# Performance work log

Hardware: AMD Instinct MI355X
Metric: run time of the kernel (lower is better)

## Reference

```python
import jax, jax.numpy as jnp
import numpy as np

EPS = 1e-5

def _bn(x, g, b):
    # training-mode BatchNorm3d over (N, T, H, W) per channel (axis=1), biased variance
    red = (0, 2, 3, 4)
    m = x.mean(red, keepdims=True)
    v = x.var(red, keepdims=True)
    s = (1, -1, 1, 1, 1)
    return (x - m) / jnp.sqrt(v + EPS) * g.reshape(s) + b.reshape(s)

def _conv3d(x, w, b):
    # Conv3d kernel (1,3,3), padding (0,1,1)
    y = jax.lax.conv_general_dilated(x, w, (1, 1, 1), ((0, 0), (1, 1), (1, 1)),
                                     dimension_numbers=('NCDHW', 'OIDHW', 'NCDHW'))
    return y + b[None, :, None, None, None]

def _forward(x1, x2, attn_weight, W_up, b_up, W_mlp, b_mlp, g_mlp, be_mlp,
             W_c1, b_c1, g_c1, be_c1, W_c2, b_c2, g_c2, be_c2):
    w2 = W_up[:, :, 0]  # [Cin, Cout, 2, 2]
    y = jnp.einsum('bcthw,cokl->bothkwl', x1, w2)
    b_, o, t, h, k, w_, l = y.shape
    x1u = y.reshape(b_, o, t, h * k, w_ * l) + b_up[None, :, None, None, None]

    bs, d_in, T, H, W = x2.shape
    nH = attn_weight.shape[0]
    hh, ww = attn_weight.shape[2], attn_weight.shape[3]
    # [nH, bs, h, w, T, T] -> [nH*bs, T*T, h, w], bilinear upsample to (H, W)
    A = attn_weight.transpose(0, 1, 4, 5, 2, 3).reshape(nH * bs, T * T, hh, ww)
    A = jax.image.resize(A, (nH * bs, T * T, H, W), method='linear')
    A = A.reshape(nH, bs, T, T, H, W)
    # per-(head,b,H,W) temporal attention matmul: avoids materializing x2.repeat(n_head,...)
    ctx = jnp.einsum('nbtsxy,bcsxy->btxycn', A, x2)  # [bs,T,H,W,d_in,nH]
    ctx = ctx.reshape(bs, T, H, W, d_in * nH)        # flatten order (c, n) matches torch permute+view
    hmlp = jnp.einsum('btxyk,ko->btxyo', ctx, W_mlp) + b_mlp
    hmlp = hmlp.transpose(0, 4, 1, 2, 3)  # [bs, enc, T, H, W]
    hmlp = jax.nn.relu(_bn(hmlp, g_mlp, be_mlp))

    x = jnp.concatenate([hmlp, x1u], axis=1)  # [bs, enc+dec, T, H, W]
    x = jax.nn.relu(_bn(_conv3d(x, W_c1, b_c1), g_c1, be_c1))
    x = jax.nn.relu(_bn(_conv3d(x, W_c2, b_c2), g_c2, be_c2))
    return x

def setup_inputs() -> dict:
    key = jax.random.key(0)
    ks = jax.random.split(key, 8)
    bs, T, H, W = 2, 8, 128, 128
    dec, enc, nH = 64, 32, 4
    hh = ww = 16  # attn_scale_factor = 8
    return {
        'x1': jax.random.normal(ks[0], (bs, dec, T, H // 2, W // 2), jnp.float32),
        'x2': jax.random.normal(ks[1], (bs, enc, T, H, W), jnp.float32),
        'attn_weight': jax.random.uniform(ks[2], (nH, bs, hh, ww, T, T), jnp.float32),
        'W_up': jax.random.normal(ks[3], (dec, dec, 1, 2, 2), jnp.float32) * 0.05,
        'b_up': jnp.zeros((dec,), jnp.float32),
        'W_mlp': jax.random.normal(ks[4], (nH * enc, enc), jnp.float32) * 0.05,
        'b_mlp': jnp.zeros((enc,), jnp.float32),
        'g_mlp': jnp.ones((enc,), jnp.float32),
        'be_mlp': jnp.zeros((enc,), jnp.float32),
        'W_c1': jax.random.normal(ks[5], (enc, dec + enc, 1, 3, 3), jnp.float32) * 0.05,
        'b_c1': jnp.zeros((enc,), jnp.float32),
        'g_c1': jnp.ones((enc,), jnp.float32),
        'be_c1': jnp.zeros((enc,), jnp.float32),
        'W_c2': jax.random.normal(ks[6], (enc, enc, 1, 3, 3), jnp.float32) * 0.05,
        'b_c2': jnp.zeros((enc,), jnp.float32),
        'g_c2': jnp.ones((enc,), jnp.float32),
        'be_c2': jnp.zeros((enc,), jnp.float32),
    }

def reference(x1, x2, attn_weight, W_up, b_up, W_mlp, b_mlp, g_mlp, be_mlp,
              W_c1, b_c1, g_c1, be_c1, W_c2, b_c2, g_c2, be_c2):
    return _forward(x1, x2, attn_weight, W_up, b_up, W_mlp, b_mlp, g_mlp, be_mlp,
                    W_c1, b_c1, g_c1, be_c1, W_c2, b_c2, g_c2, be_c2)
```

## Files before the change

### kernel.cpp

```cpp
#include <hip/hip_runtime.h>


#define EPSV 1e-5f

typedef __attribute__((ext_vector_type(8))) short short8;
typedef __attribute__((ext_vector_type(4))) short short4v;
typedef __attribute__((ext_vector_type(4))) float floatx4;

__device__ inline short f2bf(float f) {
  union { float f; unsigned u; } v; v.f = f;
  unsigned r = (v.u + 0x7fffu + ((v.u >> 16) & 1u)) >> 16;
  return (short)r;
}
__device__ inline float bf2f(short s) {
  union { unsigned u; float f; } v; v.u = ((unsigned)(unsigned short)s) << 16;
  return v.f;
}

#define UB_OFF   0
#define HMB_OFF  8388608
#define C1B_OFF  12582912
#define C2B_OFF  16777216
#define WB1_OFF  20971520
#define WB2_OFF  20985344
#define WUP_OFF  20989952
#define WMB_OFF  20998144
#define ST_OFF   21000192

__global__ __launch_bounds__(256) void k_repackb(const float* __restrict__ Wc1, const float* __restrict__ Wc2,
        const float* __restrict__ Wup, const float* __restrict__ Wmlp,
        short* __restrict__ wb1, short* __restrict__ wb2, short* __restrict__ wupb, short* __restrict__ wmb) {
  int i = blockIdx.x*256 + threadIdx.x;
  if (i < 27648) {
    int cc = i / 9216, r = i % 9216;
    int tap = r / 1024, r2 = r % 1024;
    int nt = r2 >> 9, lane = (r2 >> 3) & 63, j = r2 & 7;
    int o = nt*16 + (lane & 15);
    int cin = cc*32 + (lane >> 4)*8 + j;
    wb1[i] = f2bf(Wc1[(o*96 + cin)*9 + tap]);
  }
  if (i < 9216) {
    int tap = i / 1024, r2 = i % 1024;
    int nt = r2 >> 9, lane = (r2 >> 3) & 63, j = r2 & 7;
    int o = nt*16 + (lane & 15);
    int cin = (lane >> 4)*8 + j;
    wb2[i] = f2bf(Wc2[(o*32 + cin)*9 + tap]);
  }
  if (i < 16384) {
    int j = i & 7, lane = (i >> 3) & 63, r = i >> 9;
    int nt = r & 3, kb = (r >> 2) & 1, p = r >> 3;
    int c = kb*32 + (lane >> 4)*8 + j;
    int o = nt*16 + (lane & 15);
    wupb[i] = f2bf(Wup[(c*64 + o)*4 + p]);
  }
  if (i < 4096) {
    int j = i & 7, lane = (i >> 3) & 63, nt = (i >> 9) & 1, ck = i >> 10;
    int k = ck*32 + (lane >> 4)*8 + j;
    int o = nt*16 + (lane & 15);
    wmb[i] = f2bf(Wmlp[k*32 + o]);
  }
}

__global__ __launch_bounds__(256) void k_up(const float* __restrict__ x1,
        const short* __restrict__ wupb, const float* __restrict__ bup,
        short* __restrict__ Ub) {
  __shared__ __align__(16) char smem[34816];
  int bid = blockIdx.x;
  int tid = threadIdx.x;
  int cp = bid & 63, t = (bid >> 6) & 7, b = bid >> 9;
  int chunk = cp >> 2, parity = cp & 3;
  int lane = tid & 63, w = tid >> 6;
  short8* stage = (short8*)smem;
  {
    const float* xp = x1 + ((long)(b*64)*8 + t)*4096 + chunk*256 + tid;
    #pragma unroll
    for (int o8 = 0; o8 < 8; ++o8) {
      short8 v;
      #pragma unroll
      for (int j = 0; j < 8; ++j) v[j] = f2bf(xp[(long)(o8*8+j)*32768]);
      int kb = o8 >> 2, cq = o8 & 3;
      stage[(kb*16 + (tid>>4))*64 + cq*16 + (tid&15)] = v;
    }
  }
  __syncthreads();

  floatx4 acc[4][4];
  #pragma unroll
  for (int nt=0; nt<4; ++nt) {
    float bb = bup[nt*16 + (lane&15)];
    #pragma unroll
    for (int mt=0; mt<4; ++mt) acc[mt][nt] = (floatx4){bb,bb,bb,bb};
  }
  const short8* wp = (const short8*)wupb;
  #pragma unroll
  for (int kb=0; kb<2; ++kb) {
    short8 bfr[4];
    #pragma unroll
    for (int nt=0; nt<4; ++nt) bfr[nt] = wp[((parity*2+kb)*4+nt)*64 + lane];
    #pragma unroll
    for (int mt=0; mt<4; ++mt) {
      short8 a = stage[(kb*16 + w*4 + mt)*64 + lane];
      #pragma unroll
      for (int nt=0; nt<4; ++nt)
        acc[mt][nt] = __builtin_amdgcn_mfma_f32_16x16x32_bf16(a, bfr[nt], acc[mt][nt], 0,0,0);
    }
  }

  __syncthreads();
  short* trb = (short*)smem;
  #pragma unroll
  for (int mt=0; mt<4; ++mt)
    #pragma unroll
    for (int nt=0; nt<4; ++nt)
      #pragma unroll
      for (int r=0; r<4; ++r)
        trb[(w*64 + mt*16 + (lane>>4)*4 + r)*68 + nt*16 + (lane&15)] = f2bf(acc[mt][nt][r]);
  __syncthreads();

  int ip = chunk*256 + tid;
  int X = 2*(ip>>6) + (parity>>1), Y = 2*(ip&63) + (parity&1);
  short* dst = Ub + (((long)(b*8+t)*16384 + X*128 + Y)*64);
  const short* src = trb + tid*68;
  #pragma unroll
  for (int k=0; k<16; ++k)
    *(short4v*)(dst + k*4) = *(const short4v*)(src + k*4);
}

__global__ __launch_bounds__(256) void k_ctxmlp(const float* __restrict__ x2,
        const float* __restrict__ attn, const short* __restrict__ wmb,
        const float* __restrict__ bmlp, short* __restrict__ HMb, float* __restrict__ st) {
  __shared__ float la[2048];
  __shared__ __align__(16) short ctxs[256*40];
  __shared__ float sb[64];
  int t = blockIdx.y, b = blockIdx.z;
  int tid = threadIdx.x, lane = tid & 63, w = tid >> 6;
  int m = lane & 15, kg = lane >> 4;
  int pos = blockIdx.x*256 + tid;
  if (tid < 64) sb[tid] = 0.f;

  int x0 = blockIdx.x*2;
  int ixbase = max((int)floorf((x0+0.5f)*0.125f - 0.5f), 0);

  float4* la4 = (float4*)la;
  const float4* g4 = (const float4*)attn;
  #pragma unroll
  for (int k=0;k<2;++k) {
    int f = k*256 + tid;
    int s4 = f & 1, iy = (f>>1)&15, slot = (f>>5)&3, n = f>>7;
    int ixs = min(ixbase + slot, 15);
    la4[f] = g4[((((n*2+b)*16+ixs)*16+iy)*8+t)*2 + s4];
  }
  __syncthreads();

  int x = pos >> 7, y = pos & 127;
  float ux = (x+0.5f)*0.125f - 0.5f;
  float uy = (y+0.5f)*0.125f - 0.5f;
  int ix0 = (int)floorf(ux), iy0 = (int)floorf(uy);
  float fx = ux - (float)ix0, fy = uy - (float)iy0;
  int sa  = max(ix0,0) - ixbase;
  int sbl = min(ix0+1,15) - ixbase;
  int iya = max(iy0,0), iyb = min(iy0+1,15);
  float w00=(1.f-fx)*(1.f-fy), w01=(1.f-fx)*fy, w10=fx*(1.f-fy), w11=fx*fy;
  float a[4][8];
  #pragma unroll
  for (int n=0;n<4;++n) {
    const float4* p00 = la4 + ((n*4+sa )*16+iya)*2;
    const float4* p01 = la4 + ((n*4+sa )*16+iyb)*2;
    const float4* p10 = la4 + ((n*4+sbl)*16+iya)*2;
    const float4* p11 = la4 + ((n*4+sbl)*16+iyb)*2;
    #pragma unroll
    for (int q=0;q<2;++q) {
      float4 c00=p00[q], c01=p01[q], c10=p10[q], c11=p11[q];
      a[n][q*4+0] = w00*c00.x + w01*c01.x + w10*c10.x + w11*c11.x;
      a[n][q*4+1] = w00*c00.y + w01*c01.y + w10*c10.y + w11*c11.y;
      a[n][q*4+2] = w00*c00.z + w01*c01.z + w10*c10.z + w11*c11.z;
      a[n][q*4+3] = w00*c00.w + w01*c01.w + w10*c10.w + w11*c11.w;
    }
  }

  float b0v = bmlp[m], b1v = bmlp[16+m];
  floatx4 acc[4][2];
  #pragma unroll
  for (int mt=0; mt<4; ++mt) {
    acc[mt][0] = (floatx4){b0v,b0v,b0v,b0v};
    acc[mt][1] = (floatx4){b1v,b1v,b1v,b1v};
  }

  const short8* wm = (const short8*)wmb;
  const float* x2p = x2 + (long)b*4194304 + pos;
  for (int ck=0; ck<4; ++ck) {
    float ctx[8][4];
    #pragma unroll
    for (int c=0;c<8;++c) { ctx[c][0]=0.f; ctx[c][1]=0.f; ctx[c][2]=0.f; ctx[c][3]=0.f; }
    #pragma unroll
    for (int s=0;s<8;++s) {
      float a0=a[0][s], a1=a[1][s], a2=a[2][s], a3=a[3][s];
      #pragma unroll
      for (int c=0;c<8;++c) {
        float xv = x2p[(long)((ck*8+c)*8 + s)*16384];
        ctx[c][0] = fmaf(a0, xv, ctx[c][0]);
        ctx[c][1] = fmaf(a1, xv, ctx[c][1]);
        ctx[c][2] = fmaf(a2, xv, ctx[c][2]);
        ctx[c][3] = fmaf(a3, xv, ctx[c][3]);
      }
    }
    #pragma unroll
    for (int g=0; g<4; ++g) {
      short8 v;
      #pragma unroll
      for (int j=0;j<8;++j) { int kl = g*8+j; v[j] = f2bf(ctx[kl>>2][kl&3]); }
      *(short8*)(ctxs + tid*40 + g*8) = v;
    }
    __syncthreads();
    short8 wb0 = wm[(ck*2+0)*64 + lane];
    short8 wb1f = wm[(ck*2+1)*64 + lane];
    #pragma unroll
    for (int mt=0; mt<4; ++mt) {
      short8 af = *(const short8*)(ctxs + ((w*4+mt)*16 + m)*40 + kg*8);
      acc[mt][0] = __builtin_amdgcn_mfma_f32_16x16x32_bf16(af, wb0,  acc[mt][0], 0,0,0);
      acc[mt][1] = __builtin_amdgcn_mfma_f32_16x16x32_bf16(af, wb1f, acc[mt][1], 0,0,0);
    }
    __syncthreads();
  }

  float s0=0.f,q0=0.f,s1=0.f,q1=0.f;
  #pragma unroll
  for (int mt=0; mt<4; ++mt)
    #pragma unroll
    for (int r=0; r<4; ++r) {
      float v0 = acc[mt][0][r]; s0 += v0; q0 += v0*v0;
      float v1 = acc[mt][1][r]; s1 += v1; q1 += v1*v1;
    }
  s0 += __shfl_xor(s0,16); s0 += __shfl_xor(s0,32);
  q0 += __shfl_xor(q0,16); q0 += __shfl_xor(q0,32);
  s1 += __shfl_xor(s1,16); s1 += __shfl_xor(s1,32);
  q1 += __shfl_xor(q1,16); q1 += __shfl_xor(q1,32);
  if (lane < 16) {
    atomicAdd(&sb[lane],    s0); atomicAdd(&sb[16+lane], s1);
    atomicAdd(&sb[32+lane], q0); atomicAdd(&sb[48+lane], q1);
  }

  short* tr = ctxs;
  #pragma unroll
  for (int mt=0; mt<4; ++mt) {
    int tile = w*4 + mt;
    #pragma unroll
    for (int nt=0; nt<2; ++nt)
      #pragma unroll
      for (int r=0; r<4; ++r)
        tr[(tile*16 + kg*4 + r)*32 + nt*16 + m] = f2bf(acc[mt][nt][r]);
  }
  __syncthreads();
  long slab = (long)(b*8+t)*16384;
  short8* d8 = (short8*)(HMb + (slab + blockIdx.x*256 + tid)*32);
  const short8* s8 = (const short8*)(tr + tid*32);
  d8[0]=s8[0]; d8[1]=s8[1]; d8[2]=s8[2]; d8[3]=s8[3];
  if (tid < 64) atomicAdd(&st[tid], sb[tid]);
}

template<int NCHUNK>
__global__ __launch_bounds__(256) void k_convp(
    const short* __restrict__ src0, const short* __restrict__ srcU,
    const short* __restrict__ wb, const float* __restrict__ bias,
    const float* __restrict__ stIn, const float* __restrict__ gam,
    const float* __restrict__ bet,
    short* __restrict__ dstCL, float* __restrict__ stOut) {
  __shared__ __align__(16) short stage[324*40];
  __shared__ float sbuf[64];
  __shared__ float scs[32], shs[32];
  int t = blockIdx.y, b = blockIdx.z;
  int tid = threadIdx.x, lane = tid & 63, w = tid >> 6;
  if (tid < 64) sbuf[tid] = 0.f;
  if (tid < 32) {
    float mean = stIn[tid] * (1.f/262144.f);
    float var  = stIn[32+tid] * (1.f/262144.f) - mean*mean;
    float s = gam[tid] / sqrtf(var + EPSV);
    scs[tid] = s;
    shs[tid] = bet[tid] - mean*s;
  }
  long slab = (long)(b*8+t)*16384;
  int x0 = (int)(blockIdx.x >> 3) * 16, y0 = (int)(blockIdx.x & 7) * 16;
  int m = lane & 15, kg = lane >> 4;

  int pA = tid;        int rA = pA/18, cA = pA - rA*18;
  int XA = x0-1+rA, YA = y0-1+cA;
  bool okA = ((unsigned)XA < 128u) & ((unsigned)YA < 128u);
  int pB = tid + 256;  bool hasB = pB < 324;
  int rB = pB/18, cB = pB - rB*18;
  int XB = x0-1+rB, YB = y0-1+cB;
  bool okB = hasB && (((unsigned)XB < 128u) & ((unsigned)YB < 128u));
  long offA = slab + XA*128 + YA, offB = slab + XB*128 + YB;

  short8 preA[4], preB[4];

  float bias0 = bias[m], bias1 = bias[16 + m];
  floatx4 acc[4][2];
  #pragma unroll
  for (int mt=0; mt<4; ++mt) {
    acc[mt][0] = (floatx4){bias0,bias0,bias0,bias0};
    acc[mt][1] = (floatx4){bias1,bias1,bias1,bias1};
  }

  {
    const short* sA = src0 + offA*32;
    const short* sB = src0 + offB*32;
    #pragma unroll
    for (int g=0; g<4; ++g) {
      preA[g] = okA ? *(const short8*)(sA + g*8) : (short8)0;
      preB[g] = okB ? *(const short8*)(sB + g*8) : (short8)0;
    }
  }
  __syncthreads();
  #pragma unroll
  for (int g=0; g<4; ++g) {
    short8 vA, vB;
    #pragma unroll
    for (int j=0;j<8;++j) {
      int ch = g*8+j;
      float scv = scs[ch], shv = shs[ch];
      vA[j] = okA ? f2bf(fmaxf(fmaf(bf2f(preA[g][j]), scv, shv), 0.f)) : (short)0;
      vB[j] = okB ? f2bf(fmaxf(fmaf(bf2f(preB[g][j]), scv, shv), 0.f)) : (short)0;
    }
    *(short8*)(&stage[pA*40 + g*8]) = vA;
    if (hasB) *(short8*)(&stage[pB*40 + g*8]) = vB;
  }
  __syncthreads();

  const short8* wbp = (const short8*)wb;
  #pragma unroll
  for (int cc=0; cc<NCHUNK; ++cc) {
    short8 Bf0[9], Bf1[9];
    #pragma unroll
    for (int tap=0; tap<9; ++tap) {
      Bf0[tap] = wbp[((cc*9+tap)*2+0)*64 + lane];
      Bf1[tap] = wbp[((cc*9+tap)*2+1)*64 + lane];
    }
    if (cc+1 < NCHUNK) {
      int coff = cc*32;
      const short* sA = srcU + offA*64 + coff;
      const short* sB = srcU + offB*64 + coff;
      #pragma unroll
      for (int g=0; g<4; ++g) {
        preA[g] = okA ? *(const short8*)(sA + g*8) : (short8)0;
        preB[g] = okB ? *(const short8*)(sB + g*8) : (short8)0;
      }
    }
    #pragma unroll
    for (int tap=0; tap<9; ++tap) {
      int dy = tap/3, dx = tap - 3*dy;
      #pragma unroll
      for (int mt=0; mt<4; ++mt) {
        int p = (w*4 + mt + dy)*18 + m + dx;
        short8 a = *(const short8*)(&stage[p*40 + kg*8]);
        acc[mt][0] = __builtin_amdgcn_mfma_f32_16x16x32_bf16(a, Bf0[tap], acc[mt][0], 0,0,0);
        acc[mt][1] = __builtin_amdgcn_mfma_f32_16x16x32_bf16(a, Bf1[tap], acc[mt][1], 0,0,0);
      }
    }
    if (cc+1 < NCHUNK) {
      __syncthreads();
      #pragma unroll
      for (int g=0; g<4; ++g) {
        *(short8*)(&stage[pA*40 + g*8]) = preA[g];
        if (hasB) *(short8*)(&stage[pB*40 + g*8]) = preB[g];
      }
      __syncthreads();
    }
  }

  float s0=0.f,q0=0.f,s1=0.f,q1=0.f;
  #pragma unroll
  for (int mt=0; mt<4; ++mt)
    #pragma unroll
    for (int r=0; r<4; ++r) {
      float v0 = acc[mt][0][r]; s0 += v0; q0 += v0*v0;
      float v1 = acc[mt][1][r]; s1 += v1; q1 += v1*v1;
    }
  s0 += __shfl_xor(s0,16); s0 += __shfl_xor(s0,32);
  q0 += __shfl_xor(q0,16); q0 += __shfl_xor(q0,32);
  s1 += __shfl_xor(s1,16); s1 += __shfl_xor(s1,32);
  q1 += __shfl_xor(q1,16); q1 += __shfl_xor(q1,32);
  if (lane < 16) {
    atomicAdd(&sbuf[lane],    s0); atomicAdd(&sbuf[16+lane], s1);
    atomicAdd(&sbuf[32+lane], q0); atomicAdd(&sbuf[48+lane], q1);
  }

  __syncthreads();
  short* tr = &stage[0];
  #pragma unroll
  for (int mt=0; mt<4; ++mt) {
    int tile = w*4 + mt;
    #pragma unroll
    for (int nt=0; nt<2; ++nt)
      #pragma unroll
      for (int r=0; r<4; ++r)
        tr[(tile*16 + kg*4 + r)*32 + nt*16 + m] = f2bf(acc[mt][nt][r]);
  }
  __syncthreads();
  int px = tid >> 4, py = tid & 15;
  short8* d8 = (short8*)(dstCL + ((slab + (long)(x0+px)*128 + (y0+py))*32));
  const short8* s8 = (const short8*)(tr + tid*32);
  d8[0]=s8[0]; d8[1]=s8[1]; d8[2]=s8[2]; d8[3]=s8[3];
  if (tid < 64) atomicAdd(&stOut[tid], sbuf[tid]);
}

__global__ __launch_bounds__(256) void k_bnrelu2(const short* __restrict__ C2b,
        const float* __restrict__ stIn, const float* __restrict__ gam,
        const float* __restrict__ bet, float* __restrict__ out) {
  __shared__ float tb[10592];
  __shared__ float scs[32], shs[32];
  int t = blockIdx.y, b = blockIdx.z;
  int posbase = blockIdx.x * 256;
  int tid = threadIdx.x;
  if (tid < 32) {
    float mean = stIn[tid] * (1.f/262144.f);
    float var  = stIn[32+tid] * (1.f/262144.f) - mean*mean;
    float s = gam[tid] / sqrtf(var + EPSV);
    scs[tid] = s;
    shs[tid] = bet[tid] - mean*s;
  }
  long slab = (long)(b*8+t)*16384;
  const short8* sp = (const short8*)(C2b + (slab + posbase + tid)*32);
  short8 v[4];
  #pragma unroll
  for (int g=0; g<4; ++g) v[g] = sp[g];
  __syncthreads();
  {
    int pi = tid + (tid>>5)*8;
    #pragma unroll
    for (int g=0; g<4; ++g) {
      #pragma unroll
      for (int j=0; j<8; ++j) {
        int ch = g*8+j;
        tb[ch*321 + pi] = fmaxf(fmaf(bf2f(v[g][j]), scs[ch], shs[ch]), 0.f);
      }
    }
  }
  __syncthreads();
  int ch = tid >> 3, pg = tid & 7;
  float* op = out + ((long)(b*32+ch)*8 + t)*16384 + posbase + pg*32;
  const float* tp = tb + ch*321 + pg*40;
  #pragma unroll
  for (int k=0; k<8; ++k) {
    float4 vv;
    vv.x = tp[k*4+0]; vv.y = tp[k*4+1]; vv.z = tp[k*4+2]; vv.w = tp[k*4+3];
    *(float4*)(op + k*4) = vv;
  }
}

extern "C" void kernel_launch(void* const* d_in, const int* in_sizes, int n_in,
                              void* d_out, int out_size, void* d_ws, size_t ws_size,
                              hipStream_t stream) {
  (void)in_sizes; (void)n_in; (void)out_size; (void)ws_size;
  const float* x1   = (const float*)d_in[0];
  const float* x2   = (const float*)d_in[1];
  const float* attn = (const float*)d_in[2];
  const float* Wup  = (const float*)d_in[3];
  const float* bup  = (const float*)d_in[4];
  const float* Wmlp = (const float*)d_in[5];
  const float* bmlp = (const float*)d_in[6];
  const float* gmlp = (const float*)d_in[7];
  const float* bemlp= (const float*)d_in[8];
  const float* Wc1  = (const float*)d_in[9];
  const float* bc1  = (const float*)d_in[10];
  const float* gc1  = (const float*)d_in[11];
  const float* bec1 = (const float*)d_in[12];
  const float* Wc2  = (const float*)d_in[13];
  const float* bc2  = (const float*)d_in[14];
  const float* gc2  = (const float*)d_in[15];
  const float* bec2 = (const float*)d_in[16];
  float* ws  = (float*)d_ws;
  float* out = (float*)d_out;

  short* Ub   = (short*)(ws + UB_OFF);
  short* HMb  = (short*)(ws + HMB_OFF);
  short* C1b  = (short*)(ws + C1B_OFF);
  short* C2b  = (short*)(ws + C2B_OFF);
  short* wb1  = (short*)(ws + WB1_OFF);
  short* wb2  = (short*)(ws + WB2_OFF);
  short* wupb = (short*)(ws + WUP_OFF);
  short* wmb  = (short*)(ws + WMB_OFF);
  float* st1  = ws + ST_OFF;
  float* st2  = st1 + 64;
  float* st3  = st2 + 64;

  hipMemsetAsync(st1, 0, 192*sizeof(float), stream);
  k_repackb<<<108, 256, 0, stream>>>(Wc1, Wc2, Wup, Wmlp, wb1, wb2, wupb, wmb);
  k_up<<<1024, 256, 0, stream>>>(x1, wupb, bup, Ub);
  k_ctxmlp<<<dim3(64,8,2), 256, 0, stream>>>(x2, attn, wmb, bmlp, HMb, st1);
  k_convp<3><<<dim3(64,8,2), 256, 0, stream>>>(HMb, Ub, wb1, bc1, st1, gmlp, bemlp, C1b, st2);
  k_convp<1><<<dim3(64,8,2), 256, 0, stream>>>(C1b, nullptr, wb2, bc2, st2, gc1, bec1, C2b, st3);
  k_bnrelu2<<<dim3(64,8,2), 256, 0, stream>>>(C2b, st3, gc2, bec2, out);
}
```

Before: 312.1 us.

## Pre-transpose x2 to channel-last bf16 inside upsample kernel for ctxmlp loads

Adds an extra block range to the upsample kernel, renamed k_pre, that converts x2 to bf16 and transposes it to a position-major, channel-last layout in workspace. The context/MLP kernel then reads eight contiguous channels per time step with 16-byte vector loads instead of many strided scalar fp32 loads. This costs an extra pass over x2 (a read plus a half-size write) and rounds x2 to bf16 before the attention contraction, which adds a small precision loss.

```diff
diff --git a/kernel.cpp b/kernel.cpp
--- a/kernel.cpp
+++ b/kernel.cpp
@@ -21,11 +21,12 @@
 #define HMB_OFF  8388608
 #define C1B_OFF  12582912
 #define C2B_OFF  16777216
-#define WB1_OFF  20971520
-#define WB2_OFF  20985344
-#define WUP_OFF  20989952
-#define WMB_OFF  20998144
-#define ST_OFF   21000192
+#define X2T_OFF  20971520
+#define WB1_OFF  29360128
+#define WB2_OFF  29373952
+#define WUP_OFF  29378560
+#define WMB_OFF  29386752
+#define ST_OFF   29388800
 
 __global__ __launch_bounds__(256) void k_repackb(const float* __restrict__ Wc1, const float* __restrict__ Wc2,
         const float* __restrict__ Wup, const float* __restrict__ Wmlp,
@@ -61,12 +62,37 @@
   }
 }
 
-__global__ __launch_bounds__(256) void k_up(const float* __restrict__ x1,
+__global__ __launch_bounds__(256) void k_pre(const float* __restrict__ x1,
+        const float* __restrict__ x2,
         const short* __restrict__ wupb, const float* __restrict__ bup,
-        short* __restrict__ Ub) {
+        short* __restrict__ Ub, short* __restrict__ x2t) {
   __shared__ __align__(16) char smem[34816];
   int bid = blockIdx.x;
   int tid = threadIdx.x;
+  if (bid >= 1024) {
+    int bid2 = bid - 1024;
+    int tile = bid2 & 63, s = (bid2 >> 6) & 7, b = bid2 >> 9;
+    short* lds = (short*)smem;
+    #pragma unroll
+    for (int k=0; k<8; ++k) {
+      int f4 = k*256 + tid;
+      int c = f4 >> 6, p4 = f4 & 63;
+      float4 v = *(const float4*)(x2 + ((long)(b*32+c)*8 + s)*16384 + tile*256 + p4*4);
+      short4v o;
+      o[0]=f2bf(v.x); o[1]=f2bf(v.y); o[2]=f2bf(v.z); o[3]=f2bf(v.w);
+      *(short4v*)(lds + c*264 + p4*4) = o;
+    }
+    __syncthreads();
+    short* dst = x2t + (((long)(b*8+s)*16384) + tile*256 + tid)*32;
+    #pragma unroll
+    for (int g=0; g<4; ++g) {
+      short8 v;
+      #pragma unroll
+      for (int j=0; j<8; ++j) v[j] = lds[(g*8+j)*264 + tid];
+      *(short8*)(dst + g*8) = v;
+    }
+    return;
+  }
   int cp = bid & 63, t = (bid >> 6) & 7, b = bid >> 9;
   int chunk = cp >> 2, parity = cp & 3;
   int lane = tid & 63, w = tid >> 6;
@@ -126,7 +152,7 @@
     *(short4v*)(dst + k*4) = *(const short4v*)(src + k*4);
 }
 
-__global__ __launch_bounds__(256) void k_ctxmlp(const float* __restrict__ x2,
+__global__ __launch_bounds__(256) void k_ctxmlp(const short* __restrict__ x2t,
         const float* __restrict__ attn, const short* __restrict__ wmb,
         const float* __restrict__ bmlp, short* __restrict__ HMb, float* __restrict__ st) {
   __shared__ float la[2048];
@@ -187,8 +213,11 @@
   }
 
   const short8* wm = (const short8*)wmb;
-  const float* x2p = x2 + (long)b*4194304 + pos;
   for (int ck=0; ck<4; ++ck) {
+    short8 xr[8];
+    #pragma unroll
+    for (int s=0;s<8;++s)
+      xr[s] = *(const short8*)(x2t + (((long)(b*8+s)*16384) + pos)*32 + ck*8);
     float ctx[8][4];
     #pragma unroll
     for (int c=0;c<8;++c) { ctx[c][0]=0.f; ctx[c][1]=0.f; ctx[c][2]=0.f; ctx[c][3]=0.f; }
@@ -197,7 +226,7 @@
       float a0=a[0][s], a1=a[1][s], a2=a[2][s], a3=a[3][s];
       #pragma unroll
       for (int c=0;c<8;++c) {
-        float xv = x2p[(long)((ck*8+c)*8 + s)*16384];
+        float xv = bf2f(xr[s][c]);
         ctx[c][0] = fmaf(a0, xv, ctx[c][0]);
         ctx[c][1] = fmaf(a1, xv, ctx[c][1]);
         ctx[c][2] = fmaf(a2, xv, ctx[c][2]);
@@ -475,6 +504,7 @@
   short* HMb  = (short*)(ws + HMB_OFF);
   short* C1b  = (short*)(ws + C1B_OFF);
   short* C2b  = (short*)(ws + C2B_OFF);
+  short* x2t  = (short*)(ws + X2T_OFF);
   short* wb1  = (short*)(ws + WB1_OFF);
   short* wb2  = (short*)(ws + WB2_OFF);
   short* wupb = (short*)(ws + WUP_OFF);
@@ -485,8 +515,8 @@
 
   hipMemsetAsync(st1, 0, 192*sizeof(float), stream);
   k_repackb<<<108, 256, 0, stream>>>(Wc1, Wc2, Wup, Wmlp, wb1, wb2, wupb, wmb);
-  k_up<<<1024, 256, 0, stream>>>(x1, wupb, bup, Ub);
-  k_ctxmlp<<<dim3(64,8,2), 256, 0, stream>>>(x2, attn, wmb, bmlp, HMb, st1);
+  k_pre<<<2048, 256, 0, stream>>>(x1, x2, wupb, bup, Ub, x2t);
+  k_ctxmlp<<<dim3(64,8,2), 256, 0, stream>>>(x2t, attn, wmb, bmlp, HMb, st1);
   k_convp<3><<<dim3(64,8,2), 256, 0, stream>>>(HMb, Ub, wb1, bc1, st1, gmlp, bemlp, C1b, st2);
   k_convp<1><<<dim3(64,8,2), 256, 0, stream>>>(C1b, nullptr, wb2, bc2, st2, gc1, bec1, C2b, st3);
   k_bnrelu2<<<dim3(64,8,2), 256, 0, stream>>>(C2b, st3, gc2, bec2, out);
```

Measured after the change: 293.6 us. -5.9%, faster.
